# Optimization experiments

Hardware: AMD Instinct MI355X
Metric: run time of the kernel (lower is better)

Reference implementation:

```python
import jax, jax.numpy as jnp
import numpy as np

D_MODEL = 1024
NUM_HEADS = 16
GROUP_SIZE = 4
NUM_GROUPS = NUM_HEADS // GROUP_SIZE  # 4
D_K = D_MODEL // NUM_HEADS            # 64
THETA = 10000.0
WINDOW = 512


def _rope(x, positions):
    # x: (..., t, d) with d even; interleaved-pair rotation, freq_i = theta^{-i/(d/2)}
    d = x.shape[-1]
    half = d // 2
    inv_freq = THETA ** (-jnp.arange(half, dtype=x.dtype) / half)          # (half,)
    ang = positions.astype(x.dtype)[:, None] * inv_freq[None, :]           # (t, half)
    cos, sin = jnp.cos(ang), jnp.sin(ang)
    x1, x2 = x[..., 0::2], x[..., 1::2]
    r1 = x1 * cos - x2 * sin
    r2 = x1 * sin + x2 * cos
    return jnp.stack([r1, r2], axis=-1).reshape(x.shape)


def setup_inputs() -> dict:
    key = jax.random.key(0)
    k1, k2, k3, k4, k5 = jax.random.split(key, 5)
    b, t = 2, 2048
    scale = 1.0 / np.sqrt(D_MODEL)
    return {
        "x": jax.random.normal(k1, (b, t, D_MODEL), dtype=jnp.float32),
        "WQ": jax.random.normal(k2, (D_MODEL, D_MODEL), dtype=jnp.float32) * scale,
        "WK": jax.random.normal(k3, (NUM_GROUPS * D_K, D_MODEL), dtype=jnp.float32) * scale,
        "WV": jax.random.normal(k4, (NUM_GROUPS * D_K, D_MODEL), dtype=jnp.float32) * scale,
        "WO": jax.random.normal(k5, (D_MODEL, D_MODEL), dtype=jnp.float32) * scale,
        "token_positions": jnp.arange(t, dtype=jnp.int32),
    }


def reference(x, WQ, WK, WV, WO, token_positions):
    b, t, _ = x.shape
    g, s, d = NUM_GROUPS, GROUP_SIZE, D_K
    # projections (Linear: y = x @ W^T, no bias)
    q = (x @ WQ.T).reshape(b, t, g, s, d).transpose(0, 2, 3, 1, 4)  # b g s t d
    k = (x @ WK.T).reshape(b, t, g, d).transpose(0, 2, 1, 3)        # b g t d
    v = (x @ WV.T).reshape(b, t, g, d).transpose(0, 2, 1, 3)        # b g t d
    q = _rope(q, token_positions)
    k = _rope(k, token_positions)
    # scores: kv heads shared across the s query heads of each group
    scores = jnp.einsum('bgsqd,bgkd->bgsqk', q, k) / jnp.sqrt(jnp.asarray(d, x.dtype))
    i = jnp.arange(t)[:, None]
    j = jnp.arange(t)[None, :]
    allowed = (i >= j) & (i - j <= WINDOW)  # causal sliding window
    scores = jnp.where(allowed, scores, -jnp.inf)
    probs = jax.nn.softmax(scores, axis=-1)
    out = jnp.einsum('bgsqk,bgkd->bgsqd', probs, v)                 # b g s t d
    out = out.transpose(0, 3, 1, 2, 4).reshape(b, t, D_MODEL)       # b t (g s d)
    return out @ WO.T
```

## Files before the change

kernel.cpp:

```cpp
#include <hip/hip_runtime.h>
#include <hip/hip_bf16.h>

typedef __bf16 bf16;
typedef __bf16 bf16x4 __attribute__((ext_vector_type(4)));
typedef __bf16 bf16x8 __attribute__((ext_vector_type(8)));
typedef float  floatx4 __attribute__((ext_vector_type(4)));

#define D_MODEL   1024
#define NUM_HEADS 16
#define NUM_GROUPS 4
#define DK        64
#define SEQ_T     2048
#define BATCH     2
#define M_ROWS    (BATCH*SEQ_T)
#define WINDOW    512
#define KV_DIM    (NUM_GROUPS*DK)
#define N_QKV     (D_MODEL + 2*KV_DIM)
#define QSCALE    0.1803368801111204f
#define FREQ_C    0.4152410118609203f

#define GLDS16(g, l)                                                          \
    __builtin_amdgcn_global_load_lds(                                         \
        (const __attribute__((address_space(1))) void*)(g),                   \
        (__attribute__((address_space(3))) void*)(l), 16, 0, 0)

__global__ __launch_bounds__(256)
void convert_all(const float* s0, bf16* d0, int c0,
                 const float* s1, bf16* d1, int c1,
                 const float* s2, bf16* d2, int c2,
                 const float* s3, bf16* d3, int c3,
                 const float* s4, bf16* d4, int c4)
{
    int id = blockIdx.x * 256 + threadIdx.x;
    const float* src; bf16* dst;
    if      (id < c0)         { src = s0; dst = d0; }
    else if ((id -= c0) < c1) { src = s1; dst = d1; }
    else if ((id -= c1) < c2) { src = s2; dst = d2; }
    else if ((id -= c2) < c3) { src = s3; dst = d3; }
    else if ((id -= c3) < c4) { src = s4; dst = d4; }
    else return;
    int i = id * 8;
    const float* s = src + i;
    float4 a = *(const float4*)s;
    float4 b = *(const float4*)(s + 4);
    bf16x8 v;
    v[0] = (bf16)a.x; v[1] = (bf16)a.y; v[2] = (bf16)a.z; v[3] = (bf16)a.w;
    v[4] = (bf16)b.x; v[5] = (bf16)b.y; v[6] = (bf16)b.z; v[7] = (bf16)b.w;
    *(bf16x8*)&dst[i] = v;
}

__global__ __launch_bounds__(256, 3)
void gemm_t64(const bf16* __restrict__ A, const bf16* __restrict__ W, int K,
              bf16* __restrict__ Cq, bf16* __restrict__ Ck, bf16* __restrict__ Vt,
              float* __restrict__ Co, const int* __restrict__ pos, int mode)
{
    __shared__ bf16 As[2][128 * 64];
    __shared__ bf16 Bs[2][64 * 64];

    const int tid  = threadIdx.x;
    const int wave = tid >> 6;
    const int lane = tid & 63;
    const int lr   = lane & 15;
    const int quad = lane >> 4;
    const int m0 = blockIdx.y * 128;
    const int n0 = blockIdx.x * 64;
    const int wm = (wave >> 1) * 64;
    const int wn = (wave & 1) * 32;

    const int cr8 = lane >> 3;
    const int cc  = ((lane & 7) ^ cr8) * 8;
    const bf16* Ag = &A[(size_t)(m0 + cr8) * K + cc];
    const bf16* Wg = &W[(size_t)(n0 + cr8) * K + cc];

#define STAGE(buf, kk)                                                        \
    do {                                                                      \
        GLDS16(Ag + (size_t)((wave * 4 + 0) * 8) * K + (kk), &As[buf][(wave * 4 + 0) * 512]); \
        GLDS16(Ag + (size_t)((wave * 4 + 1) * 8) * K + (kk), &As[buf][(wave * 4 + 1) * 512]); \
        GLDS16(Ag + (size_t)((wave * 4 + 2) * 8) * K + (kk), &As[buf][(wave * 4 + 2) * 512]); \
        GLDS16(Ag + (size_t)((wave * 4 + 3) * 8) * K + (kk), &As[buf][(wave * 4 + 3) * 512]); \
        GLDS16(Wg + (size_t)((wave * 2 + 0) * 8) * K + (kk), &Bs[buf][(wave * 2 + 0) * 512]); \
        GLDS16(Wg + (size_t)((wave * 2 + 1) * 8) * K + (kk), &Bs[buf][(wave * 2 + 1) * 512]); \
    } while (0)

    const int ax0 = (quad ^ (lane & 7)) * 8;
    const int ax1 = ax0 ^ 32;

    floatx4 acc[4][2];
#pragma unroll
    for (int i = 0; i < 4; i++)
#pragma unroll
        for (int j = 0; j < 2; j++) acc[i][j] = (floatx4)(0.0f);

    STAGE(0, 0);
    __asm__ volatile("s_waitcnt vmcnt(0)" ::: "memory");
    __builtin_amdgcn_s_barrier();

    int cur = 0;
    for (int k0 = 0; k0 < K; k0 += 64) {
        if (k0 + 64 < K) STAGE(cur ^ 1, k0 + 64);

        bf16x8 a0[4], a1[4], b0[2], b1[2];
#pragma unroll
        for (int mi = 0; mi < 4; mi++) {
            a0[mi] = *(const bf16x8*)&As[cur][(wm + mi * 16 + lr) * 64 + ax0];
            a1[mi] = *(const bf16x8*)&As[cur][(wm + mi * 16 + lr) * 64 + ax1];
        }
#pragma unroll
        for (int ni = 0; ni < 2; ni++) {
            b0[ni] = *(const bf16x8*)&Bs[cur][(wn + ni * 16 + lr) * 64 + ax0];
            b1[ni] = *(const bf16x8*)&Bs[cur][(wn + ni * 16 + lr) * 64 + ax1];
        }

#pragma unroll
        for (int mi = 0; mi < 4; mi++)
#pragma unroll
            for (int ni = 0; ni < 2; ni++) {
                acc[mi][ni] = __builtin_amdgcn_mfma_f32_16x16x32_bf16(
                    a0[mi], b0[ni], acc[mi][ni], 0, 0, 0);
                acc[mi][ni] = __builtin_amdgcn_mfma_f32_16x16x32_bf16(
                    a1[mi], b1[ni], acc[mi][ni], 0, 0, 0);
            }

        __asm__ volatile("s_waitcnt vmcnt(0)" ::: "memory");
        __builtin_amdgcn_s_barrier();
        cur ^= 1;
    }
#undef STAGE

    if (mode == 0) {
        if (n0 >= D_MODEL + KV_DIM) {
            const int g  = (n0 - (D_MODEL + KV_DIM)) >> 6;
            const int b  = m0 >> 11;
            const int bg = b * 4 + g;
#pragma unroll
            for (int mi = 0; mi < 4; mi++) {
#pragma unroll
                for (int ni = 0; ni < 2; ni++) {
                    int d  = wn + ni * 16 + lr;
                    int t0 = (m0 & (SEQ_T - 1)) + wm + mi * 16 + quad * 4;
                    bf16x4 v;
#pragma unroll
                    for (int r = 0; r < 4; r++) v[r] = (bf16)acc[mi][ni][r];
                    *(bf16x4*)&Vt[((size_t)(bg * 64 + d)) * SEQ_T + t0] = v;
                }
            }
        } else {
            bf16* out; int ld, coff; float sc;
            if (n0 < D_MODEL) { out = Cq; ld = D_MODEL; coff = n0; sc = QSCALE; }
            else              { out = Ck; ld = KV_DIM;  coff = n0 - D_MODEL; sc = 1.0f; }
            float inv[2];
            float sgn = (lr & 1) ? 1.0f : -1.0f;
#pragma unroll
            for (int ni = 0; ni < 2; ni++) {
                int ip = (wn + ni * 16 + lr) >> 1;
                inv[ni] = exp2f(-(float)ip * FREQ_C);
            }
#pragma unroll
            for (int mi = 0; mi < 4; mi++) {
#pragma unroll
                for (int r = 0; r < 4; r++) {
                    int row = m0 + wm + mi * 16 + quad * 4 + r;
                    float p = (float)pos[row & (SEQ_T - 1)];
#pragma unroll
                    for (int ni = 0; ni < 2; ni++) {
                        float v  = acc[mi][ni][r];
                        float vp = __shfl_xor(v, 1);
                        float ang = p * inv[ni];
                        float ss, cc2;
                        __sincosf(ang, &ss, &cc2);
                        v = v * cc2 + vp * ss * sgn;
                        out[(size_t)row * ld + coff + wn + ni * 16 + lr] = (bf16)(v * sc);
                    }
                }
            }
        }
    } else {
#pragma unroll
        for (int mi = 0; mi < 4; mi++)
#pragma unroll
            for (int ni = 0; ni < 2; ni++)
#pragma unroll
                for (int r = 0; r < 4; r++) {
                    int row = m0 + wm + mi * 16 + quad * 4 + r;
                    int col = n0 + wn + ni * 16 + lr;
                    Co[(size_t)row * D_MODEL + col] = acc[mi][ni][r];
                }
    }
}

__global__ __launch_bounds__(256, 3)
void attn_mfma(const bf16* __restrict__ Q, const bf16* __restrict__ K,
               const bf16* __restrict__ Vt_g, bf16* __restrict__ AO)
{
    const int ST = 72;
    __shared__ bf16 Ks[64 * ST];
    __shared__ bf16 Vt[80 * ST];

    const int tid  = threadIdx.x;
    const int wave = tid >> 6;
    const int lane = tid & 63;
    const int lr   = lane & 15;
    const int quad = lane >> 4;
    const int bg = blockIdx.y;
    const int b = bg >> 2, g = bg & 3;
    const int h = g * 4 + wave;
    const int q0 = blockIdx.x * 32;

    bf16x8 qf[2][2];
#pragma unroll
    for (int mi = 0; mi < 2; mi++)
#pragma unroll
        for (int ks = 0; ks < 2; ks++)
            qf[mi][ks] = *(const bf16x8*)
                &Q[((size_t)(b * SEQ_T + q0 + mi * 16 + lr)) * D_MODEL
                   + h * 64 + ks * 32 + quad * 8];

    for (int i = tid; i < 15 * ST; i += 256) Vt[65 * ST + i] = (bf16)0.0f;
    if (tid < ST) Vt[64 * ST + tid] = (bf16)(tid < 64 ? 1.0f : 0.0f);

    floatx4 o[2][5];
#pragma unroll
    for (int mi = 0; mi < 2; mi++)
#pragma unroll
        for (int nt = 0; nt < 5; nt++) o[mi][nt] = (floatx4)(0.0f);

    const int t0   = (q0 >= WINDOW) ? ((q0 - WINDOW) & ~63) : 0;
    const int last = q0 & ~63;

    for (int j0 = t0; j0 <= last; j0 += 64) {
        const bool mC = (j0 == last);
        const bool mW = (q0 >= WINDOW) && (j0 == t0);
        __syncthreads();
#pragma unroll
        for (int i = 0; i < 2; i++) {
            int c = tid + i * 256;
            int row = c >> 3, col8 = (c & 7) * 8;
            *(bf16x8*)&Ks[row * ST + col8] =
                *(const bf16x8*)&K[((size_t)(b * SEQ_T + j0 + row)) * KV_DIM + g * 64 + col8];
            *(bf16x8*)&Vt[row * ST + col8] =
                *(const bf16x8*)&Vt_g[((size_t)(bg * 64 + row)) * SEQ_T + j0 + col8];
        }
        __syncthreads();

        floatx4 s2[4][2];
#pragma unroll
        for (int nt = 0; nt < 4; nt++)
#pragma unroll
            for (int mi = 0; mi < 2; mi++) s2[nt][mi] = (floatx4)(0.0f);
#pragma unroll
        for (int ks = 0; ks < 2; ks++) {
#pragma unroll
            for (int nt = 0; nt < 4; nt++) {
                bf16x8 kf = *(const bf16x8*)&Ks[(nt * 16 + lr) * ST + ks * 32 + quad * 8];
                s2[nt][0] = __builtin_amdgcn_mfma_f32_16x16x32_bf16(kf, qf[0][ks], s2[nt][0], 0, 0, 0);
                s2[nt][1] = __builtin_amdgcn_mfma_f32_16x16x32_bf16(kf, qf[1][ks], s2[nt][1], 0, 0, 0);
            }
        }

        if (mC) {
#pragma unroll
            for (int nt = 0; nt < 4; nt++)
#pragma unroll
                for (int mi = 0; mi < 2; mi++) {
                    int qi_ = q0 + mi * 16 + lr;
#pragma unroll
                    for (int r = 0; r < 4; r++) {
                        int key = j0 + nt * 16 + quad * 4 + r;
                        s2[nt][mi][r] = (key <= qi_) ? s2[nt][mi][r] : -1e30f;
                    }
                }
        } else if (mW) {
#pragma unroll
            for (int nt = 0; nt < 4; nt++)
#pragma unroll
                for (int mi = 0; mi < 2; mi++) {
                    int qi_ = q0 + mi * 16 + lr;
#pragma unroll
                    for (int r = 0; r < 4; r++) {
                        int key = j0 + nt * 16 + quad * 4 + r;
                        s2[nt][mi][r] = (qi_ - key <= WINDOW) ? s2[nt][mi][r] : -1e30f;
                    }
                }
        }

        bf16x8 pa[2][2];
#pragma unroll
        for (int mi = 0; mi < 2; mi++)
#pragma unroll
            for (int ks = 0; ks < 2; ks++)
#pragma unroll
                for (int r = 0; r < 4; r++) {
                    pa[mi][ks][r]     = (bf16)exp2f(s2[2 * ks][mi][r]);
                    pa[mi][ks][r + 4] = (bf16)exp2f(s2[2 * ks + 1][mi][r]);
                }

#pragma unroll
        for (int ks = 0; ks < 2; ks++) {
#pragma unroll
            for (int nt = 0; nt < 5; nt++) {
                const bf16* vb = &Vt[(nt * 16 + lr) * ST + ks * 32 + quad * 4];
                bf16x4 vlo = *(const bf16x4*)vb;
                bf16x4 vhi = *(const bf16x4*)(vb + 16);
                bf16x8 vf = __builtin_shufflevector(vlo, vhi, 0, 1, 2, 3, 4, 5, 6, 7);
                o[0][nt] = __builtin_amdgcn_mfma_f32_16x16x32_bf16(pa[0][ks], vf, o[0][nt], 0, 0, 0);
                o[1][nt] = __builtin_amdgcn_mfma_f32_16x16x32_bf16(pa[1][ks], vf, o[1][nt], 0, 0, 0);
            }
        }
    }

#pragma unroll
    for (int mi = 0; mi < 2; mi++)
#pragma unroll
        for (int r = 0; r < 4; r++) {
            float l = __shfl(o[mi][4][r], lane & 48);
            float invl = 1.0f / l;
            int row = q0 + mi * 16 + quad * 4 + r;
#pragma unroll
            for (int nt = 0; nt < 4; nt++)
                AO[((size_t)(b * SEQ_T + row)) * D_MODEL + h * 64 + nt * 16 + lr] =
                    (bf16)(o[mi][nt][r] * invl);
        }
}

extern "C" void kernel_launch(void* const* d_in, const int* in_sizes, int n_in,
                              void* d_out, int out_size, void* d_ws, size_t ws_size,
                              hipStream_t stream)
{
    const float* x  = (const float*)d_in[0];
    const float* WQ = (const float*)d_in[1];
    const float* WK = (const float*)d_in[2];
    const float* WV = (const float*)d_in[3];
    const float* WO = (const float*)d_in[4];
    const int*  pos = (const int*)d_in[5];

    char* ws   = (char*)d_ws;
    bf16* Qw   = (bf16*)ws;
    bf16* Kw   = (bf16*)(ws + (size_t) 8 * 1024 * 1024);
    bf16* Vt_g = (bf16*)(ws + (size_t)10 * 1024 * 1024);
    bf16* xb   = (bf16*)(ws + (size_t)12 * 1024 * 1024);
    bf16* AO   = xb;
    bf16* Wqkv = (bf16*)(ws + (size_t)20 * 1024 * 1024);
    bf16* WOb  = (bf16*)(ws + (size_t)23 * 1024 * 1024);

    const int cx = (M_ROWS * D_MODEL) / 8;
    const int cq = (D_MODEL * D_MODEL) / 8;
    const int ck = (KV_DIM * D_MODEL) / 8;
    const int ctot = cx + cq + 2 * ck + cq;
    convert_all<<<ctot / 256, 256, 0, stream>>>(
        x, xb, cx,
        WQ, Wqkv, cq,
        WK, Wqkv + (size_t)D_MODEL * D_MODEL, ck,
        WV, Wqkv + (size_t)(D_MODEL + KV_DIM) * D_MODEL, ck,
        WO, WOb, cq);

    gemm_t64<<<dim3(N_QKV / 64, M_ROWS / 128), 256, 0, stream>>>(
        xb, Wqkv, D_MODEL, Qw, Kw, Vt_g, nullptr, pos, 0);

    attn_mfma<<<dim3(SEQ_T / 32, BATCH * NUM_GROUPS), 256, 0, stream>>>(
        Qw, Kw, Vt_g, AO);

    gemm_t64<<<dim3(D_MODEL / 64, M_ROWS / 128), 256, 0, stream>>>(
        AO, WOb, D_MODEL, nullptr, nullptr, nullptr, (float*)d_out, pos, 1);
}
```

Baseline: 147.5 us.

## Fuse fp32-to-bf16 conversion into GEMM tile loads and prefetch K/V tiles in attention

Removes the separate conversion kernel. Both GEMMs now read fp32 inputs and weights straight from global memory into registers, convert them to bf16 and write them into LDS, replacing the async global-to-LDS loads. Attention now writes its output in fp32 for the output projection, and it prefetches the next K/V tile into registers while the current one is being processed. This saves one launch and the bf16 round trip, at the cost of twice the global read bytes per GEMM tile, more registers, and a synchronous register-staged pipeline in place of direct LDS loads.

```diff
diff --git a/kernel.cpp b/kernel.cpp
--- a/kernel.cpp
+++ b/kernel.cpp
@@ -16,43 +16,25 @@
 #define WINDOW    512
 #define KV_DIM    (NUM_GROUPS*DK)
 #define N_QKV     (D_MODEL + 2*KV_DIM)
+#define KDIM      1024
 #define QSCALE    0.1803368801111204f
 #define FREQ_C    0.4152410118609203f
 
-#define GLDS16(g, l)                                                          \
-    __builtin_amdgcn_global_load_lds(                                         \
-        (const __attribute__((address_space(1))) void*)(g),                   \
-        (__attribute__((address_space(3))) void*)(l), 16, 0, 0)
-
-__global__ __launch_bounds__(256)
-void convert_all(const float* s0, bf16* d0, int c0,
-                 const float* s1, bf16* d1, int c1,
-                 const float* s2, bf16* d2, int c2,
-                 const float* s3, bf16* d3, int c3,
-                 const float* s4, bf16* d4, int c4)
+static __device__ __forceinline__ bf16x8 cv8(float4 a, float4 b)
 {
-    int id = blockIdx.x * 256 + threadIdx.x;
-    const float* src; bf16* dst;
-    if      (id < c0)         { src = s0; dst = d0; }
-    else if ((id -= c0) < c1) { src = s1; dst = d1; }
-    else if ((id -= c1) < c2) { src = s2; dst = d2; }
-    else if ((id -= c2) < c3) { src = s3; dst = d3; }
-    else if ((id -= c3) < c4) { src = s4; dst = d4; }
-    else return;
-    int i = id * 8;
-    const float* s = src + i;
-    float4 a = *(const float4*)s;
-    float4 b = *(const float4*)(s + 4);
     bf16x8 v;
     v[0] = (bf16)a.x; v[1] = (bf16)a.y; v[2] = (bf16)a.z; v[3] = (bf16)a.w;
     v[4] = (bf16)b.x; v[5] = (bf16)b.y; v[6] = (bf16)b.z; v[7] = (bf16)b.w;
-    *(bf16x8*)&dst[i] = v;
+    return v;
 }
 
 __global__ __launch_bounds__(256, 3)
-void gemm_t64(const bf16* __restrict__ A, const bf16* __restrict__ W, int K,
-              bf16* __restrict__ Cq, bf16* __restrict__ Ck, bf16* __restrict__ Vt,
-              float* __restrict__ Co, const int* __restrict__ pos, int mode)
+void gemm_t64(const float* __restrict__ A,
+              const float* __restrict__ W0, const float* __restrict__ W1,
+              const float* __restrict__ W2,
+              bf16* __restrict__ Cq, bf16* __restrict__ Ck,
+              bf16* __restrict__ Vt, float* __restrict__ Co,
+              const int* __restrict__ pos, int mode)
 {
     __shared__ bf16 As[2][128 * 64];
     __shared__ bf16 Bs[2][64 * 64];
@@ -67,19 +49,43 @@
     const int wm = (wave >> 1) * 64;
     const int wn = (wave & 1) * 32;
 
+    const float* Wseg; int wrow;
+    if      (n0 < D_MODEL)          { Wseg = W0; wrow = n0; }
+    else if (n0 < D_MODEL + KV_DIM) { Wseg = W1; wrow = n0 - D_MODEL; }
+    else                            { Wseg = W2; wrow = n0 - D_MODEL - KV_DIM; }
+
     const int cr8 = lane >> 3;
     const int cc  = ((lane & 7) ^ cr8) * 8;
-    const bf16* Ag = &A[(size_t)(m0 + cr8) * K + cc];
-    const bf16* Wg = &W[(size_t)(n0 + cr8) * K + cc];
-
-#define STAGE(buf, kk)                                                        \
+    const float* Ag = &A[(size_t)(m0 + cr8) * KDIM + cc];
+    const float* Wg = &Wseg[(size_t)(wrow + cr8) * KDIM + cc];
+
+    float4 ra[6][2];
+#define LOADT(kk)                                                             \
     do {                                                                      \
-        GLDS16(Ag + (size_t)((wave * 4 + 0) * 8) * K + (kk), &As[buf][(wave * 4 + 0) * 512]); \
-        GLDS16(Ag + (size_t)((wave * 4 + 1) * 8) * K + (kk), &As[buf][(wave * 4 + 1) * 512]); \
-        GLDS16(Ag + (size_t)((wave * 4 + 2) * 8) * K + (kk), &As[buf][(wave * 4 + 2) * 512]); \
-        GLDS16(Ag + (size_t)((wave * 4 + 3) * 8) * K + (kk), &As[buf][(wave * 4 + 3) * 512]); \
-        GLDS16(Wg + (size_t)((wave * 2 + 0) * 8) * K + (kk), &Bs[buf][(wave * 2 + 0) * 512]); \
-        GLDS16(Wg + (size_t)((wave * 2 + 1) * 8) * K + (kk), &Bs[buf][(wave * 2 + 1) * 512]); \
+        _Pragma("unroll")                                                     \
+        for (int c = 0; c < 4; c++) {                                         \
+            const float* p = Ag + (size_t)((wave * 4 + c) * 8) * KDIM + (kk); \
+            ra[c][0] = *(const float4*)p;                                     \
+            ra[c][1] = *(const float4*)(p + 4);                               \
+        }                                                                     \
+        _Pragma("unroll")                                                     \
+        for (int c = 0; c < 2; c++) {                                         \
+            const float* p = Wg + (size_t)((wave * 2 + c) * 8) * KDIM + (kk); \
+            ra[4 + c][0] = *(const float4*)p;                                 \
+            ra[4 + c][1] = *(const float4*)(p + 4);                           \
+        }                                                                     \
+    } while (0)
+
+#define CVTW(buf)                                                             \
+    do {                                                                      \
+        _Pragma("unroll")                                                     \
+        for (int c = 0; c < 4; c++)                                           \
+            *(bf16x8*)&As[buf][(wave * 4 + c) * 512 + lane * 8] =             \
+                cv8(ra[c][0], ra[c][1]);                                      \
+        _Pragma("unroll")                                                     \
+        for (int c = 0; c < 2; c++)                                           \
+            *(bf16x8*)&Bs[buf][(wave * 2 + c) * 512 + lane * 8] =             \
+                cv8(ra[4 + c][0], ra[4 + c][1]);                              \
     } while (0)
 
     const int ax0 = (quad ^ (lane & 7)) * 8;
@@ -91,13 +97,14 @@
 #pragma unroll
         for (int j = 0; j < 2; j++) acc[i][j] = (floatx4)(0.0f);
 
-    STAGE(0, 0);
-    __asm__ volatile("s_waitcnt vmcnt(0)" ::: "memory");
-    __builtin_amdgcn_s_barrier();
+    LOADT(0);
+    CVTW(0);
+    __syncthreads();
 
     int cur = 0;
-    for (int k0 = 0; k0 < K; k0 += 64) {
-        if (k0 + 64 < K) STAGE(cur ^ 1, k0 + 64);
+    for (int k0 = 0; k0 < KDIM; k0 += 64) {
+        const bool nxt = (k0 + 64 < KDIM);
+        if (nxt) LOADT(k0 + 64);
 
         bf16x8 a0[4], a1[4], b0[2], b1[2];
 #pragma unroll
@@ -121,11 +128,12 @@
                     a1[mi], b1[ni], acc[mi][ni], 0, 0, 0);
             }
 
-        __asm__ volatile("s_waitcnt vmcnt(0)" ::: "memory");
-        __builtin_amdgcn_s_barrier();
+        if (nxt) CVTW(cur ^ 1);
+        __syncthreads();
         cur ^= 1;
     }
-#undef STAGE
+#undef LOADT
+#undef CVTW
 
     if (mode == 0) {
         if (n0 >= D_MODEL + KV_DIM) {
@@ -190,7 +198,7 @@
 
 __global__ __launch_bounds__(256, 3)
 void attn_mfma(const bf16* __restrict__ Q, const bf16* __restrict__ K,
-               const bf16* __restrict__ Vt_g, bf16* __restrict__ AO)
+               const bf16* __restrict__ Vt_g, float* __restrict__ AO)
 {
     const int ST = 72;
     __shared__ bf16 Ks[64 * ST];
@@ -227,19 +235,29 @@
     const int t0   = (q0 >= WINDOW) ? ((q0 - WINDOW) & ~63) : 0;
     const int last = q0 & ~63;
 
+    const int srow0 = tid >> 3,        scol0 = (tid & 7) * 8;
+    const int srow1 = (tid + 256) >> 3, scol1 = ((tid + 256) & 7) * 8;
+
+    bf16x8 kreg[2], vreg[2];
+#define LOADKV(jn)                                                            \
+    do {                                                                      \
+        kreg[0] = *(const bf16x8*)&K[((size_t)(b * SEQ_T + (jn) + srow0)) * KV_DIM + g * 64 + scol0]; \
+        vreg[0] = *(const bf16x8*)&Vt_g[((size_t)(bg * 64 + srow0)) * SEQ_T + (jn) + scol0];          \
+        kreg[1] = *(const bf16x8*)&K[((size_t)(b * SEQ_T + (jn) + srow1)) * KV_DIM + g * 64 + scol1]; \
+        vreg[1] = *(const bf16x8*)&Vt_g[((size_t)(bg * 64 + srow1)) * SEQ_T + (jn) + scol1];          \
+    } while (0)
+
+    LOADKV(t0);
+
     for (int j0 = t0; j0 <= last; j0 += 64) {
         const bool mC = (j0 == last);
         const bool mW = (q0 >= WINDOW) && (j0 == t0);
         __syncthreads();
-#pragma unroll
-        for (int i = 0; i < 2; i++) {
-            int c = tid + i * 256;
-            int row = c >> 3, col8 = (c & 7) * 8;
-            *(bf16x8*)&Ks[row * ST + col8] =
-                *(const bf16x8*)&K[((size_t)(b * SEQ_T + j0 + row)) * KV_DIM + g * 64 + col8];
-            *(bf16x8*)&Vt[row * ST + col8] =
-                *(const bf16x8*)&Vt_g[((size_t)(bg * 64 + row)) * SEQ_T + j0 + col8];
-        }
+        *(bf16x8*)&Ks[srow0 * ST + scol0] = kreg[0];
+        *(bf16x8*)&Vt[srow0 * ST + scol0] = vreg[0];
+        *(bf16x8*)&Ks[srow1 * ST + scol1] = kreg[1];
+        *(bf16x8*)&Vt[srow1 * ST + scol1] = vreg[1];
+        if (j0 + 64 <= last) LOADKV(j0 + 64);
         __syncthreads();
 
         floatx4 s2[4][2];
@@ -307,6 +325,7 @@
             }
         }
     }
+#undef LOADKV
 
 #pragma unroll
     for (int mi = 0; mi < 2; mi++)
@@ -318,7 +337,7 @@
 #pragma unroll
             for (int nt = 0; nt < 4; nt++)
                 AO[((size_t)(b * SEQ_T + row)) * D_MODEL + h * 64 + nt * 16 + lr] =
-                    (bf16)(o[mi][nt][r] * invl);
+                    o[mi][nt][r] * invl;
         }
 }
 
@@ -333,32 +352,19 @@
     const float* WO = (const float*)d_in[4];
     const int*  pos = (const int*)d_in[5];
 
-    char* ws   = (char*)d_ws;
-    bf16* Qw   = (bf16*)ws;
-    bf16* Kw   = (bf16*)(ws + (size_t) 8 * 1024 * 1024);
-    bf16* Vt_g = (bf16*)(ws + (size_t)10 * 1024 * 1024);
-    bf16* xb   = (bf16*)(ws + (size_t)12 * 1024 * 1024);
-    bf16* AO   = xb;
-    bf16* Wqkv = (bf16*)(ws + (size_t)20 * 1024 * 1024);
-    bf16* WOb  = (bf16*)(ws + (size_t)23 * 1024 * 1024);
-
-    const int cx = (M_ROWS * D_MODEL) / 8;
-    const int cq = (D_MODEL * D_MODEL) / 8;
-    const int ck = (KV_DIM * D_MODEL) / 8;
-    const int ctot = cx + cq + 2 * ck + cq;
-    convert_all<<<ctot / 256, 256, 0, stream>>>(
-        x, xb, cx,
-        WQ, Wqkv, cq,
-        WK, Wqkv + (size_t)D_MODEL * D_MODEL, ck,
-        WV, Wqkv + (size_t)(D_MODEL + KV_DIM) * D_MODEL, ck,
-        WO, WOb, cq);
+    char* ws    = (char*)d_ws;
+    bf16* Qw    = (bf16*)ws;
+    bf16* Kw    = (bf16*)(ws + (size_t) 8 * 1024 * 1024);
+    bf16* Vt_g  = (bf16*)(ws + (size_t)10 * 1024 * 1024);
+    float* AOf  = (float*)(ws + (size_t)12 * 1024 * 1024);
 
     gemm_t64<<<dim3(N_QKV / 64, M_ROWS / 128), 256, 0, stream>>>(
-        xb, Wqkv, D_MODEL, Qw, Kw, Vt_g, nullptr, pos, 0);
+        x, WQ, WK, WV, Qw, Kw, Vt_g, nullptr, pos, 0);
 
     attn_mfma<<<dim3(SEQ_T / 32, BATCH * NUM_GROUPS), 256, 0, stream>>>(
-        Qw, Kw, Vt_g, AO);
+        Qw, Kw, Vt_g, AOf);
 
     gemm_t64<<<dim3(D_MODEL / 64, M_ROWS / 128), 256, 0, stream>>>(
-        AO, WOb, D_MODEL, nullptr, nullptr, nullptr, (float*)d_out, pos, 1);
+        AOf, WO, nullptr, nullptr, nullptr, nullptr, nullptr,
+        (float*)d_out, pos, 1);
 }
```

Measured after the change: 154.2 us. +4.6%, slower.

## Load GEMM operands directly from global, remap blocks per XCD, prefetch KV in attention

Applied to the files above, without the earlier changes.

The GEMM drops its LDS double-buffered global_load_lds staging and instead reads MFMA fragments straight from global memory into registers, unrolled by two, with K fixed at compile time. The grid becomes 1-D, and block ids are remapped so that each of the 8 chiplets gets a contiguous range of tiles, aiming for better L2 reuse. The attention kernel now prefetches the next K/V tile into registers while the current tile is in LDS, to hide global latency. The cost is that GEMM operands are no longer shared through LDS, so every wave fetches its own A/B fragments with uncoalesced 16-byte strided loads, which adds global and cache traffic.

```diff
diff --git a/kernel.cpp b/kernel.cpp
--- a/kernel.cpp
+++ b/kernel.cpp
@@ -16,13 +16,9 @@
 #define WINDOW    512
 #define KV_DIM    (NUM_GROUPS*DK)
 #define N_QKV     (D_MODEL + 2*KV_DIM)
+#define KDIM      1024
 #define QSCALE    0.1803368801111204f
 #define FREQ_C    0.4152410118609203f
-
-#define GLDS16(g, l)                                                          \
-    __builtin_amdgcn_global_load_lds(                                         \
-        (const __attribute__((address_space(1))) void*)(g),                   \
-        (__attribute__((address_space(3))) void*)(l), 16, 0, 0)
 
 __global__ __launch_bounds__(256)
 void convert_all(const float* s0, bf16* d0, int c0,
@@ -49,41 +45,30 @@
     *(bf16x8*)&dst[i] = v;
 }
 
-__global__ __launch_bounds__(256, 3)
-void gemm_t64(const bf16* __restrict__ A, const bf16* __restrict__ W, int K,
-              bf16* __restrict__ Cq, bf16* __restrict__ Ck, bf16* __restrict__ Vt,
-              float* __restrict__ Co, const int* __restrict__ pos, int mode)
+__global__ __launch_bounds__(256)
+void gemm_t64(const bf16* __restrict__ A, const bf16* __restrict__ W,
+              bf16* __restrict__ Cq, bf16* __restrict__ Ck,
+              bf16* __restrict__ Vt, float* __restrict__ Co,
+              const int* __restrict__ pos, int mode)
 {
-    __shared__ bf16 As[2][128 * 64];
-    __shared__ bf16 Bs[2][64 * 64];
-
     const int tid  = threadIdx.x;
     const int wave = tid >> 6;
     const int lane = tid & 63;
     const int lr   = lane & 15;
     const int quad = lane >> 4;
-    const int m0 = blockIdx.y * 128;
-    const int n0 = blockIdx.x * 64;
+
+    const int nx    = (mode == 0) ? (N_QKV / 64) : (D_MODEL / 64);
+    const int bid   = blockIdx.x;
+    const int chunk = gridDim.x >> 3;
+    const int v     = (bid & 7) * chunk + (bid >> 3);
+    const int m0 = (v / nx) * 128;
+    const int n0 = (v % nx) * 64;
+
     const int wm = (wave >> 1) * 64;
     const int wn = (wave & 1) * 32;
 
-    const int cr8 = lane >> 3;
-    const int cc  = ((lane & 7) ^ cr8) * 8;
-    const bf16* Ag = &A[(size_t)(m0 + cr8) * K + cc];
-    const bf16* Wg = &W[(size_t)(n0 + cr8) * K + cc];
-
-#define STAGE(buf, kk)                                                        \
-    do {                                                                      \
-        GLDS16(Ag + (size_t)((wave * 4 + 0) * 8) * K + (kk), &As[buf][(wave * 4 + 0) * 512]); \
-        GLDS16(Ag + (size_t)((wave * 4 + 1) * 8) * K + (kk), &As[buf][(wave * 4 + 1) * 512]); \
-        GLDS16(Ag + (size_t)((wave * 4 + 2) * 8) * K + (kk), &As[buf][(wave * 4 + 2) * 512]); \
-        GLDS16(Ag + (size_t)((wave * 4 + 3) * 8) * K + (kk), &As[buf][(wave * 4 + 3) * 512]); \
-        GLDS16(Wg + (size_t)((wave * 2 + 0) * 8) * K + (kk), &Bs[buf][(wave * 2 + 0) * 512]); \
-        GLDS16(Wg + (size_t)((wave * 2 + 1) * 8) * K + (kk), &Bs[buf][(wave * 2 + 1) * 512]); \
-    } while (0)
-
-    const int ax0 = (quad ^ (lane & 7)) * 8;
-    const int ax1 = ax0 ^ 32;
+    const bf16* Ap = &A[(size_t)(m0 + wm + lr) * KDIM + quad * 8];
+    const bf16* Wp = &W[(size_t)(n0 + wn + lr) * KDIM + quad * 8];
 
     floatx4 acc[4][2];
 #pragma unroll
@@ -91,24 +76,20 @@
 #pragma unroll
         for (int j = 0; j < 2; j++) acc[i][j] = (floatx4)(0.0f);
 
-    STAGE(0, 0);
-    __asm__ volatile("s_waitcnt vmcnt(0)" ::: "memory");
-    __builtin_amdgcn_s_barrier();
-
-    int cur = 0;
-    for (int k0 = 0; k0 < K; k0 += 64) {
-        if (k0 + 64 < K) STAGE(cur ^ 1, k0 + 64);
-
+#pragma unroll 2
+    for (int k0 = 0; k0 < KDIM; k0 += 64) {
         bf16x8 a0[4], a1[4], b0[2], b1[2];
 #pragma unroll
         for (int mi = 0; mi < 4; mi++) {
-            a0[mi] = *(const bf16x8*)&As[cur][(wm + mi * 16 + lr) * 64 + ax0];
-            a1[mi] = *(const bf16x8*)&As[cur][(wm + mi * 16 + lr) * 64 + ax1];
+            const bf16* p = Ap + (size_t)(mi * 16) * KDIM + k0;
+            a0[mi] = *(const bf16x8*)p;
+            a1[mi] = *(const bf16x8*)(p + 32);
         }
 #pragma unroll
         for (int ni = 0; ni < 2; ni++) {
-            b0[ni] = *(const bf16x8*)&Bs[cur][(wn + ni * 16 + lr) * 64 + ax0];
-            b1[ni] = *(const bf16x8*)&Bs[cur][(wn + ni * 16 + lr) * 64 + ax1];
+            const bf16* p = Wp + (size_t)(ni * 16) * KDIM + k0;
+            b0[ni] = *(const bf16x8*)p;
+            b1[ni] = *(const bf16x8*)(p + 32);
         }
 
 #pragma unroll
@@ -120,12 +101,7 @@
                 acc[mi][ni] = __builtin_amdgcn_mfma_f32_16x16x32_bf16(
                     a1[mi], b1[ni], acc[mi][ni], 0, 0, 0);
             }
-
-        __asm__ volatile("s_waitcnt vmcnt(0)" ::: "memory");
-        __builtin_amdgcn_s_barrier();
-        cur ^= 1;
     }
-#undef STAGE
 
     if (mode == 0) {
         if (n0 >= D_MODEL + KV_DIM) {
@@ -138,10 +114,10 @@
                 for (int ni = 0; ni < 2; ni++) {
                     int d  = wn + ni * 16 + lr;
                     int t0 = (m0 & (SEQ_T - 1)) + wm + mi * 16 + quad * 4;
-                    bf16x4 v;
-#pragma unroll
-                    for (int r = 0; r < 4; r++) v[r] = (bf16)acc[mi][ni][r];
-                    *(bf16x4*)&Vt[((size_t)(bg * 64 + d)) * SEQ_T + t0] = v;
+                    bf16x4 vv;
+#pragma unroll
+                    for (int r = 0; r < 4; r++) vv[r] = (bf16)acc[mi][ni][r];
+                    *(bf16x4*)&Vt[((size_t)(bg * 64 + d)) * SEQ_T + t0] = vv;
                 }
             }
         } else {
@@ -163,13 +139,13 @@
                     float p = (float)pos[row & (SEQ_T - 1)];
 #pragma unroll
                     for (int ni = 0; ni < 2; ni++) {
-                        float v  = acc[mi][ni][r];
-                        float vp = __shfl_xor(v, 1);
+                        float vv = acc[mi][ni][r];
+                        float vp = __shfl_xor(vv, 1);
                         float ang = p * inv[ni];
                         float ss, cc2;
                         __sincosf(ang, &ss, &cc2);
-                        v = v * cc2 + vp * ss * sgn;
-                        out[(size_t)row * ld + coff + wn + ni * 16 + lr] = (bf16)(v * sc);
+                        vv = vv * cc2 + vp * ss * sgn;
+                        out[(size_t)row * ld + coff + wn + ni * 16 + lr] = (bf16)(vv * sc);
                     }
                 }
             }
@@ -227,19 +203,29 @@
     const int t0   = (q0 >= WINDOW) ? ((q0 - WINDOW) & ~63) : 0;
     const int last = q0 & ~63;
 
+    const int srow0 = tid >> 3,        scol0 = (tid & 7) * 8;
+    const int srow1 = (tid + 256) >> 3, scol1 = ((tid + 256) & 7) * 8;
+
+    bf16x8 kreg[2], vreg[2];
+#define LOADKV(jn)                                                            \
+    do {                                                                      \
+        kreg[0] = *(const bf16x8*)&K[((size_t)(b * SEQ_T + (jn) + srow0)) * KV_DIM + g * 64 + scol0]; \
+        vreg[0] = *(const bf16x8*)&Vt_g[((size_t)(bg * 64 + srow0)) * SEQ_T + (jn) + scol0];          \
+        kreg[1] = *(const bf16x8*)&K[((size_t)(b * SEQ_T + (jn) + srow1)) * KV_DIM + g * 64 + scol1]; \
+        vreg[1] = *(const bf16x8*)&Vt_g[((size_t)(bg * 64 + srow1)) * SEQ_T + (jn) + scol1];          \
+    } while (0)
+
+    LOADKV(t0);
+
     for (int j0 = t0; j0 <= last; j0 += 64) {
         const bool mC = (j0 == last);
         const bool mW = (q0 >= WINDOW) && (j0 == t0);
         __syncthreads();
-#pragma unroll
-        for (int i = 0; i < 2; i++) {
-            int c = tid + i * 256;
-            int row = c >> 3, col8 = (c & 7) * 8;
-            *(bf16x8*)&Ks[row * ST + col8] =
-                *(const bf16x8*)&K[((size_t)(b * SEQ_T + j0 + row)) * KV_DIM + g * 64 + col8];
-            *(bf16x8*)&Vt[row * ST + col8] =
-                *(const bf16x8*)&Vt_g[((size_t)(bg * 64 + row)) * SEQ_T + j0 + col8];
-        }
+        *(bf16x8*)&Ks[srow0 * ST + scol0] = kreg[0];
+        *(bf16x8*)&Vt[srow0 * ST + scol0] = vreg[0];
+        *(bf16x8*)&Ks[srow1 * ST + scol1] = kreg[1];
+        *(bf16x8*)&Vt[srow1 * ST + scol1] = vreg[1];
+        if (j0 + 64 <= last) LOADKV(j0 + 64);
         __syncthreads();
 
         floatx4 s2[4][2];
@@ -307,6 +293,7 @@
             }
         }
     }
+#undef LOADKV
 
 #pragma unroll
     for (int mi = 0; mi < 2; mi++)
@@ -353,12 +340,12 @@
         WV, Wqkv + (size_t)(D_MODEL + KV_DIM) * D_MODEL, ck,
         WO, WOb, cq);
 
-    gemm_t64<<<dim3(N_QKV / 64, M_ROWS / 128), 256, 0, stream>>>(
-        xb, Wqkv, D_MODEL, Qw, Kw, Vt_g, nullptr, pos, 0);
+    gemm_t64<<<(N_QKV / 64) * (M_ROWS / 128), 256, 0, stream>>>(
+        xb, Wqkv, Qw, Kw, Vt_g, nullptr, pos, 0);
 
     attn_mfma<<<dim3(SEQ_T / 32, BATCH * NUM_GROUPS), 256, 0, stream>>>(
         Qw, Kw, Vt_g, AO);
 
-    gemm_t64<<<dim3(D_MODEL / 64, M_ROWS / 128), 256, 0, stream>>>(
-        AO, WOb, D_MODEL, nullptr, nullptr, nullptr, (float*)d_out, pos, 1);
+    gemm_t64<<<(D_MODEL / 64) * (M_ROWS / 128), 256, 0, stream>>>(
+        AO, WOb, nullptr, nullptr, nullptr, (float*)d_out, pos, 1);
 }
```

New measurement: 216.7 us. 47.0% more time.
